# Optimization experiments

Hardware: AMD Instinct MI355X
Metric: run time of the kernel (lower is better)

## Reference

```python
import jax, jax.numpy as jnp
import numpy as np

TOP_K = 2

def setup_inputs() -> dict:
    key = jax.random.key(0)
    k0, k1, k2, k3 = jax.random.split(key, 4)
    B, S, H, I, E = 2, 2048, 1024, 1408, 8
    hidden_states = jax.random.normal(k0, (B, S, H), dtype=jnp.float32)
    router_weight = jax.random.normal(k1, (E, H), dtype=jnp.float32) * 0.02
    gate_up_proj = jax.random.normal(k2, (E, 2 * I, H), dtype=jnp.float32) * 0.02
    down_proj = jax.random.normal(k3, (E, H, I), dtype=jnp.float32) * 0.02
    return {
        "hidden_states": hidden_states,
        "router_weight": router_weight,
        "gate_up_proj": gate_up_proj,
        "down_proj": down_proj,
    }

def reference(hidden_states, router_weight, gate_up_proj, down_proj):
    B, S, H = hidden_states.shape
    E = router_weight.shape[0]
    x = hidden_states.reshape(-1, H)                       # [T, H]
    T = x.shape[0]
    # Router: logits -> float32 softmax -> top-k (matches torch: topk on probs)
    logits = x @ router_weight.T                           # [T, E]
    probs = jax.nn.softmax(logits.astype(jnp.float32), axis=-1)
    topw, topi = jax.lax.top_k(probs, TOP_K)               # [T, K]
    topw = topw.astype(x.dtype)
    # Per-token combine weights over experts (zero for non-selected experts).
    combine = jnp.zeros((T, E), dtype=x.dtype)
    combine = combine.at[jnp.arange(T)[:, None], topi].set(topw)  # [T, E]
    # Dense grouped expert compute (same math as gather-GEMM-scatter loop:
    # tokens not routed to expert e get combine weight 0).
    gu = jnp.einsum('th,eoh->teo', x, gate_up_proj)        # [T, E, 2I]
    g, u = jnp.split(gu, 2, axis=-1)                       # [T, E, I] each
    h = jax.nn.silu(g) * u                                 # [T, E, I]
    y = jnp.einsum('tei,ehi->teh', h, down_proj)           # [T, E, H]
    out = jnp.einsum('teh,te->th', y, combine)             # [T, H]
    return out.reshape(B, S, H)
```

## Files before the change

### kernel.cpp

```cpp
#include <hip/hip_runtime.h>
#include <math.h>

#define NTOK 4096
#define HDIM 1024
#define NEXP 8
#define IDIM 1408
#define TWO_I 2816
#define BM 128
#define NRB 72
#define ROWCAP (NRB * BM)

typedef _Float16 f16x8 __attribute__((ext_vector_type(8)));
typedef float f32x4 __attribute__((ext_vector_type(4)));

typedef __attribute__((address_space(1))) const unsigned int gu32;
typedef __attribute__((address_space(3))) unsigned int lu32;
__device__ __forceinline__ void async16(const void* g, void* l) {
  __builtin_amdgcn_global_load_lds((gu32*)g, (lu32*)l, 16, 0, 0);
}

__device__ __forceinline__ void seg_prefix(const int* __restrict__ counts, int* aof) {
  int o = 0; aof[0] = 0;
#pragma unroll
  for (int i = 0; i < 8; i++) { o += (counts[i] + 127) & ~127; aof[i + 1] = o; }
}

extern "C" __global__ void moe_init(int* counts, int* cursor, int* tok) {
  int i = blockIdx.x * 256 + threadIdx.x;
  if (i < NEXP) { counts[i] = 0; cursor[i] = 0; }
  if (i < ROWCAP) tok[i] = -1;
}

#define NG8 (NEXP * TWO_I * HDIM / 8)
#define ND8 (NEXP * HDIM * IDIM / 8)
extern "C" __global__ void moe_cvtw(const float* __restrict__ gup, const float* __restrict__ dp,
                                    _Float16* __restrict__ guph, _Float16* __restrict__ dph) {
  int i = blockIdx.x * 256 + threadIdx.x;
  const float4* s; uint4* d; size_t idx;
  if (i < NG8) { s = (const float4*)gup; d = (uint4*)guph; idx = i; }
  else if (i < NG8 + ND8) { s = (const float4*)dp; d = (uint4*)dph; idx = i - NG8; }
  else return;
  float4 a = s[idx * 2], b = s[idx * 2 + 1];
  union { _Float16 h[8]; uint4 u; } p;
  p.h[0] = (_Float16)a.x; p.h[1] = (_Float16)a.y; p.h[2] = (_Float16)a.z; p.h[3] = (_Float16)a.w;
  p.h[4] = (_Float16)b.x; p.h[5] = (_Float16)b.y; p.h[6] = (_Float16)b.z; p.h[7] = (_Float16)b.w;
  d[idx] = p.u;
}

extern "C" __global__ void moe_router(const float* __restrict__ x,
                                      const float* __restrict__ rw,
                                      int* __restrict__ topi,
                                      float* __restrict__ topw,
                                      _Float16* __restrict__ xh) {
  int w = threadIdx.x >> 6, lane = threadIdx.x & 63;
  int t = blockIdx.x * 4 + w;
  const float4* xp = (const float4*)(x + (size_t)t * HDIM);
  const float4* rp = (const float4*)rw;
  float acc[NEXP];
#pragma unroll
  for (int e = 0; e < NEXP; e++) acc[e] = 0.f;
#pragma unroll
  for (int i = 0; i < HDIM / 256; i++) {
    float4 xv = xp[i * 64 + lane];
    union { _Float16 h[4]; uint2 u; } pk;
    pk.h[0] = (_Float16)xv.x; pk.h[1] = (_Float16)xv.y;
    pk.h[2] = (_Float16)xv.z; pk.h[3] = (_Float16)xv.w;
    *(uint2*)(xh + (size_t)t * HDIM + i * 256 + lane * 4) = pk.u;
#pragma unroll
    for (int e = 0; e < NEXP; e++) {
      float4 rv = rp[e * 256 + i * 64 + lane];
      acc[e] += xv.x * rv.x + xv.y * rv.y + xv.z * rv.z + xv.w * rv.w;
    }
  }
#pragma unroll
  for (int e = 0; e < NEXP; e++) {
#pragma unroll
    for (int off = 32; off > 0; off >>= 1) acc[e] += __shfl_down(acc[e], off);
  }
  if (lane == 0) {
    float m = acc[0];
    for (int e = 1; e < NEXP; e++) m = fmaxf(m, acc[e]);
    float p[NEXP], s = 0.f;
    for (int e = 0; e < NEXP; e++) { p[e] = __expf(acc[e] - m); s += p[e]; }
    float inv = 1.f / s;
    int i0 = 0; float b0 = p[0];
    for (int e = 1; e < NEXP; e++) if (p[e] > b0) { b0 = p[e]; i0 = e; }
    int i1 = -1; float b1 = -1.f;
    for (int e = 0; e < NEXP; e++) if (e != i0 && p[e] > b1) { b1 = p[e]; i1 = e; }
    topi[t * 2] = i0; topi[t * 2 + 1] = i1;
    topw[t * 2] = b0 * inv; topw[t * 2 + 1] = b1 * inv;
  }
}

extern "C" __global__ void moe_count(const int* __restrict__ topi, int* __restrict__ counts) {
  __shared__ int cnt[NEXP];
  if (threadIdx.x < NEXP) cnt[threadIdx.x] = 0;
  __syncthreads();
  int t = blockIdx.x * 256 + threadIdx.x;
  atomicAdd(&cnt[topi[t * 2]], 1);
  atomicAdd(&cnt[topi[t * 2 + 1]], 1);
  __syncthreads();
  if (threadIdx.x < NEXP) atomicAdd(&counts[threadIdx.x], cnt[threadIdx.x]);
}

extern "C" __global__ void moe_scatter(const int* __restrict__ topi, const float* __restrict__ topw,
                                       const int* __restrict__ counts, int* __restrict__ cursor,
                                       int* __restrict__ tok, float* __restrict__ wrow,
                                       int* __restrict__ rows) {
  __shared__ int cnt[NEXP];
  __shared__ int base[NEXP];
  int aof[9]; seg_prefix(counts, aof);
  int tid = threadIdx.x;
  if (tid < NEXP) cnt[tid] = 0;
  __syncthreads();
  int t = blockIdx.x * 256 + tid;
  int e0 = topi[t * 2], e1 = topi[t * 2 + 1];
  int r0 = atomicAdd(&cnt[e0], 1);
  int r1 = atomicAdd(&cnt[e1], 1);
  __syncthreads();
  if (tid < NEXP) base[tid] = atomicAdd(&cursor[tid], cnt[tid]);
  __syncthreads();
  int row0 = aof[e0] + base[e0] + r0;
  int row1 = aof[e1] + base[e1] + r1;
  tok[row0] = t; wrow[row0] = topw[t * 2];     rows[t * 2]     = row0;
  tok[row1] = t; wrow[row1] = topw[t * 2 + 1]; rows[t * 2 + 1] = row1;
}

union SM1 {
  struct { _Float16 a[2][BM * 32]; _Float16 b[2][BM * 32]; } st;
  _Float16 ubuf[BM * 66];
};

extern "C" __global__ __launch_bounds__(256) void moe_gemm1(
    const _Float16* __restrict__ xh, const _Float16* __restrict__ guph,
    const int* __restrict__ counts, const int* __restrict__ tok,
    _Float16* __restrict__ hbuf) {
  __shared__ __align__(16) SM1 sm;
  int aof[9]; seg_prefix(counts, aof);
  int nl = aof[8] >> 7;
  int fid = blockIdx.x;
  int g = fid & 7, s = fid >> 3;
  int rb0 = (g * nl) >> 3, ng = (((g + 1) * nl) >> 3) - rb0;
  if (s >= ng * 22) return;
  int jl = s % 11, u = s / 11;
  int r = u % ng, jh = u / ng;
  int j = jh * 11 + jl;
  int rb = rb0 + r;
  int row0 = rb * BM;
  int e = 0;
#pragma unroll
  for (int i = 0; i < 8; i++) if (row0 >= aof[i]) e = i;

  const int tid = threadIdx.x;
  const int lane = tid & 63, w = tid >> 6;
  const int wm = w & 1, wn = w >> 1;
  const int quad = lane >> 4, l15 = lane & 15;

  f32x4 acc[4][4];
#pragma unroll
  for (int im = 0; im < 4; im++)
#pragma unroll
    for (int in = 0; in < 4; in++) acc[im][in] = (f32x4){0.f, 0.f, 0.f, 0.f};

  const int lq = lane >> 2;
  const int ls = lane & 3;
  const int gsl = ls ^ ((lq >> 1) & 3);
  const int rA0 = w * 16 + lq, rA1 = rA0 + 64;
  int tA0 = tok[row0 + rA0]; tA0 = tA0 < 0 ? 0 : tA0;
  int tA1 = tok[row0 + rA1]; tA1 = tA1 < 0 ? 0 : tA1;
  const _Float16* gA0 = xh + (size_t)tA0 * HDIM + gsl * 8;
  const _Float16* gA1 = xh + (size_t)tA1 * HDIM + gsl * 8;
  const _Float16* eb = guph + (size_t)e * TWO_I * HDIM;
  const _Float16* gB0 = eb + (size_t)(j * 64 + rA0) * HDIM + gsl * 8;
  const _Float16* gB1 = eb + (size_t)(IDIM + j * 64 + rA0) * HDIM + gsl * 8;
  _Float16* lA0k0 = &sm.st.a[0][w * 512];        _Float16* lA0k1 = &sm.st.a[1][w * 512];
  _Float16* lA1k0 = &sm.st.a[0][(w + 4) * 512];  _Float16* lA1k1 = &sm.st.a[1][(w + 4) * 512];
  _Float16* lB0k0 = &sm.st.b[0][w * 512];        _Float16* lB0k1 = &sm.st.b[1][w * 512];
  _Float16* lB1k0 = &sm.st.b[0][(w + 4) * 512];  _Float16* lB1k1 = &sm.st.b[1][(w + 4) * 512];

  const int qsw = (quad ^ ((l15 >> 1) & 3)) * 8;

  for (int kb = 0; kb < HDIM / 64; kb++) {
    async16(gA0, lA0k0); async16(gA0 + 32, lA0k1);
    async16(gA1, lA1k0); async16(gA1 + 32, lA1k1);
    async16(gB0, lB0k0); async16(gB0 + 32, lB0k1);
    async16(gB1, lB1k0); async16(gB1 + 32, lB1k1);
    gA0 += 64; gA1 += 64; gB0 += 64; gB1 += 64;
    __syncthreads();
#pragma unroll
    for (int kh = 0; kh < 2; kh++) {
      f16x8 av[4], bv[4];
#pragma unroll
      for (int im = 0; im < 4; im++)
        av[im] = *(const f16x8*)&sm.st.a[kh][(wm * 64 + im * 16 + l15) * 32 + qsw];
#pragma unroll
      for (int in = 0; in < 4; in++)
        bv[in] = *(const f16x8*)&sm.st.b[kh][(wn * 64 + in * 16 + l15) * 32 + qsw];
#pragma unroll
      for (int im = 0; im < 4; im++)
#pragma unroll
        for (int in = 0; in < 4; in++)
          acc[im][in] = __builtin_amdgcn_mfma_f32_16x16x32_f16(av[im], bv[in], acc[im][in], 0, 0, 0);
    }
    __syncthreads();
  }

  if (wn == 1) {
#pragma unroll
    for (int im = 0; im < 4; im++)
#pragma unroll
      for (int in = 0; in < 4; in++)
#pragma unroll
        for (int r2 = 0; r2 < 4; r2++)
          sm.ubuf[(wm * 64 + im * 16 + quad * 4 + r2) * 66 + in * 16 + l15] = (_Float16)acc[im][in][r2];
  }
  __syncthreads();
  if (wn == 0) {
#pragma unroll
    for (int im = 0; im < 4; im++)
#pragma unroll
      for (int in = 0; in < 4; in++)
#pragma unroll
        for (int r2 = 0; r2 < 4; r2++) {
          float gg = acc[im][in][r2];
          float uu = (float)sm.ubuf[(wm * 64 + im * 16 + quad * 4 + r2) * 66 + in * 16 + l15];
          float hh = gg / (1.f + __expf(-gg)) * uu;
          int row = row0 + wm * 64 + im * 16 + quad * 4 + r2;
          hbuf[(size_t)row * IDIM + j * 64 + in * 16 + l15] = (_Float16)hh;
        }
  }
}

extern "C" __global__ __launch_bounds__(256) void moe_gemm2(
    const _Float16* __restrict__ hbuf, const _Float16* __restrict__ dph,
    const int* __restrict__ counts, const float* __restrict__ wrow,
    _Float16* __restrict__ yh) {
  __shared__ __align__(16) struct { _Float16 a[2][BM * 32]; _Float16 b[2][BM * 32]; } sm;
  int aof[9]; seg_prefix(counts, aof);
  int nl = aof[8] >> 7;
  int fid = blockIdx.x;
  int g = fid & 7, s = fid >> 3;
  int rb0 = (g * nl) >> 3, ng = (((g + 1) * nl) >> 3) - rb0;
  if (s >= ng * 8) return;
  int cb = s & 7, r = s >> 3;
  int rb = rb0 + r;
  int row0 = rb * BM;
  int e = 0;
#pragma unroll
  for (int i = 0; i < 8; i++) if (row0 >= aof[i]) e = i;

  const int tid = threadIdx.x;
  const int lane = tid & 63, w = tid >> 6;
  const int wm = w & 1, wn = w >> 1;
  const int quad = lane >> 4, l15 = lane & 15;

  f32x4 acc[4][4];
#pragma unroll
  for (int im = 0; im < 4; im++)
#pragma unroll
    for (int in = 0; in < 4; in++) acc[im][in] = (f32x4){0.f, 0.f, 0.f, 0.f};

  const int lq = lane >> 2, ls = lane & 3;
  const int gsl = ls ^ ((lq >> 1) & 3);
  const int rA0 = w * 16 + lq;
  const _Float16* gA0 = hbuf + (size_t)(row0 + rA0) * IDIM + gsl * 8;
  const _Float16* gA1 = gA0 + (size_t)64 * IDIM;
  const _Float16* eb = dph + (size_t)e * HDIM * IDIM;
  const _Float16* gB0 = eb + (size_t)(cb * 128 + rA0) * IDIM + gsl * 8;
  const _Float16* gB1 = gB0 + (size_t)64 * IDIM;
  _Float16* lA0k0 = &sm.a[0][w * 512];        _Float16* lA0k1 = &sm.a[1][w * 512];
  _Float16* lA1k0 = &sm.a[0][(w + 4) * 512];  _Float16* lA1k1 = &sm.a[1][(w + 4) * 512];
  _Float16* lB0k0 = &sm.b[0][w * 512];        _Float16* lB0k1 = &sm.b[1][w * 512];
  _Float16* lB1k0 = &sm.b[0][(w + 4) * 512];  _Float16* lB1k1 = &sm.b[1][(w + 4) * 512];

  const int qsw = (quad ^ ((l15 >> 1) & 3)) * 8;

  for (int kb = 0; kb < IDIM / 64; kb++) {
    async16(gA0, lA0k0); async16(gA0 + 32, lA0k1);
    async16(gA1, lA1k0); async16(gA1 + 32, lA1k1);
    async16(gB0, lB0k0); async16(gB0 + 32, lB0k1);
    async16(gB1, lB1k0); async16(gB1 + 32, lB1k1);
    gA0 += 64; gA1 += 64; gB0 += 64; gB1 += 64;
    __syncthreads();
#pragma unroll
    for (int kh = 0; kh < 2; kh++) {
      f16x8 av[4], bv[4];
#pragma unroll
      for (int im = 0; im < 4; im++)
        av[im] = *(const f16x8*)&sm.a[kh][(wm * 64 + im * 16 + l15) * 32 + qsw];
#pragma unroll
      for (int in = 0; in < 4; in++)
        bv[in] = *(const f16x8*)&sm.b[kh][(wn * 64 + in * 16 + l15) * 32 + qsw];
#pragma unroll
      for (int im = 0; im < 4; im++)
#pragma unroll
        for (int in = 0; in < 4; in++)
          acc[im][in] = __builtin_amdgcn_mfma_f32_16x16x32_f16(av[im], bv[in], acc[im][in], 0, 0, 0);
    }
    __syncthreads();
  }

#pragma unroll
  for (int im = 0; im < 4; im++) {
#pragma unroll
    for (int r2 = 0; r2 < 4; r2++) {
      int row = row0 + wm * 64 + im * 16 + quad * 4 + r2;
      float wgt = wrow[row];
#pragma unroll
      for (int in = 0; in < 4; in++) {
        int col = cb * 128 + wn * 64 + in * 16 + l15;
        yh[(size_t)row * HDIM + col] = (_Float16)(acc[im][in][r2] * wgt);
      }
    }
  }
}

extern "C" __global__ void moe_combine(const _Float16* __restrict__ yh,
                                       const int* __restrict__ rows,
                                       float* __restrict__ out) {
  int i = blockIdx.x * 256 + threadIdx.x;
  int t = i >> 7, c8 = i & 127;
  int rA = rows[t * 2], rB = rows[t * 2 + 1];
  union { uint4 u; _Float16 h[8]; } pa, pb;
  pa.u = ((const uint4*)(yh + (size_t)rA * HDIM))[c8];
  pb.u = ((const uint4*)(yh + (size_t)rB * HDIM))[c8];
  float4 o0, o1;
  o0.x = (float)pa.h[0] + (float)pb.h[0]; o0.y = (float)pa.h[1] + (float)pb.h[1];
  o0.z = (float)pa.h[2] + (float)pb.h[2]; o0.w = (float)pa.h[3] + (float)pb.h[3];
  o1.x = (float)pa.h[4] + (float)pb.h[4]; o1.y = (float)pa.h[5] + (float)pb.h[5];
  o1.z = (float)pa.h[6] + (float)pb.h[6]; o1.w = (float)pa.h[7] + (float)pb.h[7];
  ((float4*)out)[(size_t)i * 2] = o0;
  ((float4*)out)[(size_t)i * 2 + 1] = o1;
}

extern "C" void kernel_launch(void* const* d_in, const int* in_sizes, int n_in,
                              void* d_out, int out_size, void* d_ws, size_t ws_size,
                              hipStream_t stream) {
  const float* x   = (const float*)d_in[0];
  const float* rw  = (const float*)d_in[1];
  const float* gup = (const float*)d_in[2];
  const float* dp  = (const float*)d_in[3];
  float* out = (float*)d_out;

  char* ws = (char*)d_ws;
  int*   counts = (int*)ws;
  int*   cursor = (int*)(ws + 64);
  int*   topi   = (int*)(ws + 4096);
  float* topw   = (float*)(ws + 36864);
  int*   tok    = (int*)(ws + 69632);
  float* wrow   = (float*)(ws + 106496);
  int*   rows   = (int*)(ws + 143360);
  _Float16* xh   = (_Float16*)(ws + 176128);
  _Float16* guph = (_Float16*)(ws + 8564736);
  _Float16* dph  = (_Float16*)(ws + 54702080);
  _Float16* hbuf = (_Float16*)(ws + 77770752);
  _Float16* yh   = (_Float16*)(ws + 103723008);

  moe_init<<<(ROWCAP + 255) / 256, 256, 0, stream>>>(counts, cursor, tok);
  moe_router<<<NTOK / 4, 256, 0, stream>>>(x, rw, topi, topw, xh);
  moe_count<<<NTOK / 256, 256, 0, stream>>>(topi, counts);
  moe_scatter<<<NTOK / 256, 256, 0, stream>>>(topi, topw, counts, cursor, tok, wrow, rows);
  moe_cvtw<<<(NG8 + ND8 + 255) / 256, 256, 0, stream>>>(gup, dp, guph, dph);
  moe_gemm1<<<8 * 22 * 9, 256, 0, stream>>>(xh, guph, counts, tok, hbuf);
  moe_gemm2<<<8 * 8 * 9, 256, 0, stream>>>(hbuf, dph, counts, wrow, yh);
  moe_combine<<<NTOK * HDIM / 8 / 256, 256, 0, stream>>>(yh, rows, out);
}
```

Before: 341.4 us.

## Replace direct-to-LDS async loads with register-staged double-buffered pipeline in both GEMMs

Both expert GEMM kernels stop using global_load_lds with a load-then-sync-then-compute loop over 64-wide K blocks. They now prefetch 32-wide K slices into registers, write them to the alternate LDS buffer while the current one is consumed by MFMAs, and sync once per step. The goal is to overlap global memory latency with compute. The cost is extra VGPRs, explicit LDS store instructions, and twice as many barriers, since each step covers half the K.

```diff
diff --git a/kernel.cpp b/kernel.cpp
--- a/kernel.cpp
+++ b/kernel.cpp
@@ -12,12 +12,6 @@
 
 typedef _Float16 f16x8 __attribute__((ext_vector_type(8)));
 typedef float f32x4 __attribute__((ext_vector_type(4)));
-
-typedef __attribute__((address_space(1))) const unsigned int gu32;
-typedef __attribute__((address_space(3))) unsigned int lu32;
-__device__ __forceinline__ void async16(const void* g, void* l) {
-  __builtin_amdgcn_global_load_lds((gu32*)g, (lu32*)l, 16, 0, 0);
-}
 
 __device__ __forceinline__ void seg_prefix(const int* __restrict__ counts, int* aof) {
   int o = 0; aof[0] = 0;
@@ -173,36 +167,52 @@
   const _Float16* eb = guph + (size_t)e * TWO_I * HDIM;
   const _Float16* gB0 = eb + (size_t)(j * 64 + rA0) * HDIM + gsl * 8;
   const _Float16* gB1 = eb + (size_t)(IDIM + j * 64 + rA0) * HDIM + gsl * 8;
-  _Float16* lA0k0 = &sm.st.a[0][w * 512];        _Float16* lA0k1 = &sm.st.a[1][w * 512];
-  _Float16* lA1k0 = &sm.st.a[0][(w + 4) * 512];  _Float16* lA1k1 = &sm.st.a[1][(w + 4) * 512];
-  _Float16* lB0k0 = &sm.st.b[0][w * 512];        _Float16* lB0k1 = &sm.st.b[1][w * 512];
-  _Float16* lB1k0 = &sm.st.b[0][(w + 4) * 512];  _Float16* lB1k1 = &sm.st.b[1][(w + 4) * 512];
-
+
+  const int c0 = w * 512 + lane * 8;
+  const int c1 = (w + 4) * 512 + lane * 8;
   const int qsw = (quad ^ ((l15 >> 1) & 3)) * 8;
 
-  for (int kb = 0; kb < HDIM / 64; kb++) {
-    async16(gA0, lA0k0); async16(gA0 + 32, lA0k1);
-    async16(gA1, lA1k0); async16(gA1 + 32, lA1k1);
-    async16(gB0, lB0k0); async16(gB0 + 32, lB0k1);
-    async16(gB1, lB1k0); async16(gB1 + 32, lB1k1);
-    gA0 += 64; gA1 += 64; gB0 += 64; gB1 += 64;
-    __syncthreads();
-#pragma unroll
-    for (int kh = 0; kh < 2; kh++) {
-      f16x8 av[4], bv[4];
-#pragma unroll
-      for (int im = 0; im < 4; im++)
-        av[im] = *(const f16x8*)&sm.st.a[kh][(wm * 64 + im * 16 + l15) * 32 + qsw];
+  uint4 rgA0, rgA1, rgB0, rgB1;
+  auto gload = [&]() {
+    rgA0 = *(const uint4*)gA0; rgA1 = *(const uint4*)gA1;
+    rgB0 = *(const uint4*)gB0; rgB1 = *(const uint4*)gB1;
+    gA0 += 32; gA1 += 32; gB0 += 32; gB1 += 32;
+  };
+  auto swrite = [&](int ph) {
+    _Float16* ab = &sm.st.a[ph][0]; _Float16* bb = &sm.st.b[ph][0];
+    *(uint4*)(ab + c0) = rgA0; *(uint4*)(ab + c1) = rgA1;
+    *(uint4*)(bb + c0) = rgB0; *(uint4*)(bb + c1) = rgB1;
+  };
+  auto compute = [&](int ph) {
+    const _Float16* ab = &sm.st.a[ph][0]; const _Float16* bb = &sm.st.b[ph][0];
+    f16x8 av[4], bv[4];
+#pragma unroll
+    for (int im = 0; im < 4; im++)
+      av[im] = *(const f16x8*)&ab[(wm * 64 + im * 16 + l15) * 32 + qsw];
+#pragma unroll
+    for (int in = 0; in < 4; in++)
+      bv[in] = *(const f16x8*)&bb[(wn * 64 + in * 16 + l15) * 32 + qsw];
+#pragma unroll
+    for (int im = 0; im < 4; im++)
 #pragma unroll
       for (int in = 0; in < 4; in++)
-        bv[in] = *(const f16x8*)&sm.st.b[kh][(wn * 64 + in * 16 + l15) * 32 + qsw];
-#pragma unroll
-      for (int im = 0; im < 4; im++)
-#pragma unroll
-        for (int in = 0; in < 4; in++)
-          acc[im][in] = __builtin_amdgcn_mfma_f32_16x16x32_f16(av[im], bv[in], acc[im][in], 0, 0, 0);
+        acc[im][in] = __builtin_amdgcn_mfma_f32_16x16x32_f16(av[im], bv[in], acc[im][in], 0, 0, 0);
+  };
+
+  const int KS = HDIM / 32;
+  gload();
+  swrite(0);
+  gload();
+  __syncthreads();
+  int cur = 0;
+  for (int k = 0; k < KS; k++) {
+    compute(cur);
+    if (k + 1 < KS) {
+      swrite(cur ^ 1);
+      if (k + 2 < KS) gload();
     }
     __syncthreads();
+    cur ^= 1;
   }
 
   if (wn == 1) {
@@ -268,36 +278,52 @@
   const _Float16* eb = dph + (size_t)e * HDIM * IDIM;
   const _Float16* gB0 = eb + (size_t)(cb * 128 + rA0) * IDIM + gsl * 8;
   const _Float16* gB1 = gB0 + (size_t)64 * IDIM;
-  _Float16* lA0k0 = &sm.a[0][w * 512];        _Float16* lA0k1 = &sm.a[1][w * 512];
-  _Float16* lA1k0 = &sm.a[0][(w + 4) * 512];  _Float16* lA1k1 = &sm.a[1][(w + 4) * 512];
-  _Float16* lB0k0 = &sm.b[0][w * 512];        _Float16* lB0k1 = &sm.b[1][w * 512];
-  _Float16* lB1k0 = &sm.b[0][(w + 4) * 512];  _Float16* lB1k1 = &sm.b[1][(w + 4) * 512];
-
+
+  const int c0 = w * 512 + lane * 8;
+  const int c1 = (w + 4) * 512 + lane * 8;
   const int qsw = (quad ^ ((l15 >> 1) & 3)) * 8;
 
-  for (int kb = 0; kb < IDIM / 64; kb++) {
-    async16(gA0, lA0k0); async16(gA0 + 32, lA0k1);
-    async16(gA1, lA1k0); async16(gA1 + 32, lA1k1);
-    async16(gB0, lB0k0); async16(gB0 + 32, lB0k1);
-    async16(gB1, lB1k0); async16(gB1 + 32, lB1k1);
-    gA0 += 64; gA1 += 64; gB0 += 64; gB1 += 64;
-    __syncthreads();
-#pragma unroll
-    for (int kh = 0; kh < 2; kh++) {
-      f16x8 av[4], bv[4];
-#pragma unroll
-      for (int im = 0; im < 4; im++)
-        av[im] = *(const f16x8*)&sm.a[kh][(wm * 64 + im * 16 + l15) * 32 + qsw];
+  uint4 rgA0, rgA1, rgB0, rgB1;
+  auto gload = [&]() {
+    rgA0 = *(const uint4*)gA0; rgA1 = *(const uint4*)gA1;
+    rgB0 = *(const uint4*)gB0; rgB1 = *(const uint4*)gB1;
+    gA0 += 32; gA1 += 32; gB0 += 32; gB1 += 32;
+  };
+  auto swrite = [&](int ph) {
+    _Float16* ab = &sm.a[ph][0]; _Float16* bb = &sm.b[ph][0];
+    *(uint4*)(ab + c0) = rgA0; *(uint4*)(ab + c1) = rgA1;
+    *(uint4*)(bb + c0) = rgB0; *(uint4*)(bb + c1) = rgB1;
+  };
+  auto compute = [&](int ph) {
+    const _Float16* ab = &sm.a[ph][0]; const _Float16* bb = &sm.b[ph][0];
+    f16x8 av[4], bv[4];
+#pragma unroll
+    for (int im = 0; im < 4; im++)
+      av[im] = *(const f16x8*)&ab[(wm * 64 + im * 16 + l15) * 32 + qsw];
+#pragma unroll
+    for (int in = 0; in < 4; in++)
+      bv[in] = *(const f16x8*)&bb[(wn * 64 + in * 16 + l15) * 32 + qsw];
+#pragma unroll
+    for (int im = 0; im < 4; im++)
 #pragma unroll
       for (int in = 0; in < 4; in++)
-        bv[in] = *(const f16x8*)&sm.b[kh][(wn * 64 + in * 16 + l15) * 32 + qsw];
-#pragma unroll
-      for (int im = 0; im < 4; im++)
-#pragma unroll
-        for (int in = 0; in < 4; in++)
-          acc[im][in] = __builtin_amdgcn_mfma_f32_16x16x32_f16(av[im], bv[in], acc[im][in], 0, 0, 0);
+        acc[im][in] = __builtin_amdgcn_mfma_f32_16x16x32_f16(av[im], bv[in], acc[im][in], 0, 0, 0);
+  };
+
+  const int KS = IDIM / 32;
+  gload();
+  swrite(0);
+  gload();
+  __syncthreads();
+  int cur = 0;
+  for (int k = 0; k < KS; k++) {
+    compute(cur);
+    if (k + 1 < KS) {
+      swrite(cur ^ 1);
+      if (k + 2 < KS) gload();
     }
     __syncthreads();
+    cur ^= 1;
   }
 
 #pragma unroll
```

Result: no change. 340.3 us (-0.3%).
